# Optimization experiments

Hardware: AMD Instinct MI355X
Metric: run time of the kernel (lower is better)

The kernel has to match this reference:

```python
import jax, jax.numpy as jnp
import numpy as np

T, B, IN, H, F, OUT = 2048, 32, 256, 512, 2048, 256


def setup_inputs() -> dict:
    key = jax.random.key(0)
    ks = jax.random.split(key, 9)
    s_in = 1.0 / np.sqrt(IN)
    s_h = 1.0 / np.sqrt(H)
    s_f = 1.0 / np.sqrt(F)
    return {
        "x": jax.random.normal(ks[0], (T, B, IN), dtype=jnp.float32),
        "Wg": jax.random.uniform(ks[1], (H, IN), jnp.float32, -s_in, s_in),
        "bg": jax.random.uniform(ks[2], (H,), jnp.float32, -s_in, s_in),
        "Wi": jax.random.uniform(ks[3], (H, IN), jnp.float32, -s_in, s_in),
        "bi": jax.random.uniform(ks[4], (H,), jnp.float32, -s_in, s_in),
        "W1": jax.random.uniform(ks[5], (F, H), jnp.float32, -s_h, s_h),
        "b1": jax.random.uniform(ks[6], (F,), jnp.float32, -s_h, s_h),
        "W2": jax.random.uniform(ks[7], (OUT, F), jnp.float32, -s_f, s_f),
        "b2": jax.random.uniform(ks[8], (OUT,), jnp.float32, -s_f, s_f),
    }


def _gilr_scan(a, b):
    # h_t = a_t * h_{t-1} + b_t with h_0 = 0  ->  parallel associative scan over time
    def combine(c1, c2):
        a1, b1 = c1
        a2, b2 = c2
        return (a1 * a2, b1 * a2 + b2)
    _, h = jax.lax.associative_scan(combine, (a, b), axis=0)
    return h


def reference(x, Wg, bg, Wi, bi, W1, b1, W2, b2):
    # x: (T, B, IN)
    g = jax.nn.sigmoid(jnp.einsum("tbi,hi->tbh", x, Wg) + bg)  # (T,B,H)
    i = jnp.tanh(jnp.einsum("tbi,hi->tbh", x, Wi) + bi)        # (T,B,H)
    h = _gilr_scan(g, (1.0 - g) * i)                             # (T,B,H)
    z = jax.nn.gelu(jnp.einsum("tbh,fh->tbf", h, W1) + b1, approximate=False)
    out = jnp.einsum("tbf,of->tbo", z, W2) + b2                  # (T,B,OUT)
    return out
```

## Files before the change

kernel.cpp:

```cpp
#include <hip/hip_runtime.h>
#include <hip/hip_fp16.h>
#include <math.h>


#define T_DIM 2048
#define B_DIM 32
#define IN_DIM 256
#define H_DIM 512
#define F_DIM 2048
#define OUT_DIM 256

typedef _Float16 f16;
typedef _Float16 f16x8 __attribute__((ext_vector_type(8)));
typedef float f32x4 __attribute__((ext_vector_type(4)));

#define AS3(p) ((__attribute__((address_space(3))) void*)(p))
#define AS1(p) ((const __attribute__((address_space(1))) void*)(p))
#define MFMA16(d, x, y) d = __builtin_amdgcn_mfma_f32_16x16x32_f16(x, y, d, 0, 0, 0)


__global__ void cvt_kernel(const float* __restrict__ in, f16* __restrict__ out, int n8) {
  int i = blockIdx.x * blockDim.x + threadIdx.x;
  if (i >= n8) return;
  const float4* p = (const float4*)in + (size_t)i * 2;
  float4 a = p[0], b = p[1];
  f16x8 o = { (f16)a.x, (f16)a.y, (f16)a.z, (f16)a.w,
              (f16)b.x, (f16)b.y, (f16)b.z, (f16)b.w };
  *((f16x8*)out + i) = o;
}

__global__ void bias_cat_kernel(const float* __restrict__ bg, const float* __restrict__ bi,
                                float* __restrict__ bgi) {
  int t = threadIdx.x;
  bgi[t] = (t < 512) ? bg[t] : bi[t - 512];
}


template <int MODE, int LN, int MPX>
__global__ __launch_bounds__(256, 2) void gemm_bt(
    const f16* __restrict__ A, const f16* __restrict__ Bw,
    const float* __restrict__ bias, void* __restrict__ Cout,
    int lda, int ldb, int ldc, int K) {
  __shared__ f16 lds[2][2][128][64];
  const int tid = threadIdx.x;
  const int wid = tid >> 6, lane = tid & 63;
  const int bid = blockIdx.x;
  const int xcd = bid & 7, loc = bid >> 3;
  const int m0 = (xcd * MPX + (loc >> LN)) * 128;
  const int n0 = (loc & ((1 << LN) - 1)) * 128;
  const int wr = (wid >> 1) * 64;
  const int wc = (wid & 1) * 64;
  const int NT = K >> 6;

  auto stage = [&](int buf, int kt) {
    const f16* ga = A + (size_t)m0 * lda + kt * 64;
    const f16* gb = Bw + (size_t)n0 * ldb + kt * 64;
    f16* la = &lds[buf][0][0][0];
    f16* lb = &lds[buf][1][0][0];
#pragma unroll
    for (int q = 0; q < 4; ++q) {
      int seg = (wid << 2) + q;
      int s = seg * 64 + lane;
      int row = s >> 3, col = (s & 7) << 3;
      __builtin_amdgcn_global_load_lds(AS1(ga + (size_t)row * lda + col),
                                       AS3(la + seg * 512), 16, 0, 0);
      __builtin_amdgcn_global_load_lds(AS1(gb + (size_t)row * ldb + col),
                                       AS3(lb + seg * 512), 16, 0, 0);
    }
  };

  f32x4 acc[4][4] = {};
  stage(0, 0);
  for (int kt = 0; kt < NT; ++kt) {
    __syncthreads();
    if (kt + 1 < NT) stage((kt + 1) & 1, kt + 1);
    f16(*At)[64] = lds[kt & 1][0];
    f16(*Bt)[64] = lds[kt & 1][1];
    const int r = lane & 15, cg = (lane >> 4) << 3;
#pragma unroll
    for (int kk = 0; kk < 2; ++kk) {
      f16x8 af[4], bf[4];
#pragma unroll
      for (int i = 0; i < 4; ++i)
        af[i] = *(const f16x8*)&At[wr + i * 16 + r][kk * 32 + cg];
#pragma unroll
      for (int i = 0; i < 4; ++i)
        bf[i] = *(const f16x8*)&Bt[wc + i * 16 + r][kk * 32 + cg];
#pragma unroll
      for (int mi = 0; mi < 4; ++mi)
#pragma unroll
        for (int ni = 0; ni < 4; ++ni)
          acc[mi][ni] = __builtin_amdgcn_mfma_f32_16x16x32_f16(af[mi], bf[ni], acc[mi][ni], 0, 0, 0);
    }
  }

  const int r = lane & 15, rq = (lane >> 4) * 4;
#pragma unroll
  for (int ni = 0; ni < 4; ++ni) {
    int col = n0 + wc + ni * 16 + r;
    float bv = bias[col];
#pragma unroll
    for (int mi = 0; mi < 4; ++mi) {
#pragma unroll
      for (int j = 0; j < 4; ++j) {
        int row = m0 + wr + mi * 16 + rq + j;
        float v = acc[mi][ni][j] + bv;
        if constexpr (MODE == 2)
          ((float*)Cout)[(size_t)row * ldc + col] = v;
        else
          ((f16*)Cout)[(size_t)row * ldc + col] = (f16)v;
      }
    }
  }
}


__device__ __forceinline__ float gelu_fast(float v) {
  float u = v * v;
  float y = v * fmaf(0.0713548353f, u, 1.59576912161f);
  float e = __expf(-y);
  return v * __builtin_amdgcn_rcpf(1.0f + e);
}

__global__ __launch_bounds__(256, 2) void gemm2_f(
    const f16* __restrict__ A, const f16* __restrict__ Bw,
    const float* __restrict__ bias, f16* __restrict__ Cout) {
  constexpr int LDA = 1024, LDB = 512, LDC = 2048, K = 512, NT = K / 32;
  __shared__ f16 lds[3][384 * 32];
  const int tid = threadIdx.x, wid = tid >> 6, lane = tid & 63;
  const int lr = lane & 15;
  const int bid = blockIdx.x;
  const int m0 = ((bid & 7) * 8 + (bid >> 7)) * 256;
  const int n0 = ((bid >> 3) & 15) * 128;
  const int wr = (wid >> 1) * 128, wc = (wid & 1) * 64;

  const f16* srcA[4];
  const f16* srcB[2];
#pragma unroll
  for (int q = 0; q < 4; ++q) {
    int s = wid * 256 + q * 64 + lane;
    int row = s >> 2, g = (s & 3) ^ ((row + (row >> 2)) & 3);
    srcA[q] = A + (size_t)(m0 + row) * LDA + g * 8;
  }
#pragma unroll
  for (int q = 0; q < 2; ++q) {
    int s = wid * 128 + q * 64 + lane;
    int row = s >> 2, g = (s & 3) ^ ((row + (row >> 2)) & 3);
    srcB[q] = Bw + (size_t)(n0 + row) * LDB + g * 8;
  }

  auto stageA = [&](int buf, int kt) {
    f16* d = lds[buf] + wid * 2048;
#pragma unroll
    for (int q = 0; q < 4; ++q)
      __builtin_amdgcn_global_load_lds(AS1(srcA[q] + kt * 32), AS3(d + q * 512), 16, 0, 0);
  };
  auto stageB = [&](int buf, int kt) {
    f16* d = lds[buf] + 8192 + wid * 1024;
#pragma unroll
    for (int q = 0; q < 2; ++q)
      __builtin_amdgcn_global_load_lds(AS1(srcB[q] + kt * 32), AS3(d + q * 512), 16, 0, 0);
  };

  const int qsf = (((lane >> 4) ^ ((lr + (lr >> 2)) & 3)) << 3);
  auto fragA = [&](int buf, int mi) -> f16x8 {
    return *(const f16x8*)(lds[buf] + (wr + mi * 16 + lr) * 32 + qsf);
  };
  auto fragB = [&](int buf, int ni) -> f16x8 {
    return *(const f16x8*)(lds[buf] + 8192 + (wc + ni * 16 + lr) * 32 + qsf);
  };

  f32x4 acc[8][4] = {};
  stageA(0, 0); stageB(0, 0);
  stageA(1, 1); stageB(1, 1);
  asm volatile("s_waitcnt vmcnt(6)" ::: "memory");
  __builtin_amdgcn_s_barrier();

#pragma unroll
  for (int kt = 0; kt < NT; ++kt) {
    const int cur = kt % 3, nx2 = (kt + 2) % 3;
    f16x8 a[8], b[4];
#pragma unroll
    for (int mi = 0; mi < 8; ++mi) a[mi] = fragA(cur, mi);
    b[0] = fragB(cur, 0);
    b[1] = fragB(cur, 1);
    if (kt + 2 < NT) stageA(nx2, kt + 2);
    __builtin_amdgcn_s_barrier();
    asm volatile("s_waitcnt lgkmcnt(0)" ::: "memory");
    __builtin_amdgcn_sched_barrier(0);
    __builtin_amdgcn_s_setprio(1);
#pragma unroll
    for (int mi = 0; mi < 8; ++mi) { MFMA16(acc[mi][0], a[mi], b[0]); MFMA16(acc[mi][1], a[mi], b[1]); }
    __builtin_amdgcn_s_setprio(0);
    __builtin_amdgcn_s_barrier();
    b[2] = fragB(cur, 2);
    b[3] = fragB(cur, 3);
    if (kt + 2 < NT) stageB(nx2, kt + 2);
    __builtin_amdgcn_s_barrier();
    asm volatile("s_waitcnt lgkmcnt(0)" ::: "memory");
    __builtin_amdgcn_sched_barrier(0);
    __builtin_amdgcn_s_setprio(1);
#pragma unroll
    for (int mi = 0; mi < 8; ++mi) { MFMA16(acc[mi][2], a[mi], b[2]); MFMA16(acc[mi][3], a[mi], b[3]); }
    __builtin_amdgcn_s_setprio(0);
    if (kt + 2 < NT) asm volatile("s_waitcnt vmcnt(6)" ::: "memory");
    else             asm volatile("s_waitcnt vmcnt(0)" ::: "memory");
    __builtin_amdgcn_s_barrier();
  }

  __syncthreads();
  f16* ep = &lds[0][0] + wid * 8192;
  const int rq = (lane >> 4) * 4;
#pragma unroll
  for (int mi = 0; mi < 8; ++mi) {
#pragma unroll
    for (int ni = 0; ni < 4; ++ni) {
      int c = ni * 2 + (lr >> 3);
      float bv = bias[n0 + wc + ni * 16 + lr];
#pragma unroll
      for (int j = 0; j < 4; ++j) {
        int row = mi * 16 + rq + j;
        float v = gelu_fast(acc[mi][ni][j] + bv);
        ep[row * 64 + ((c ^ (row & 7)) << 3) + (lr & 7)] = (f16)v;
      }
    }
  }
  asm volatile("s_waitcnt lgkmcnt(0)" ::: "memory");
  __builtin_amdgcn_sched_barrier(0);
#pragma unroll
  for (int t = 0; t < 16; ++t) {
    int idx = t * 64 + lane;
    int row = idx >> 3, c = idx & 7;
    f16x8 v = *(const f16x8*)(ep + row * 64 + ((c ^ (row & 7)) << 3));
    *(f16x8*)(Cout + (size_t)(m0 + wr + row) * LDC + (n0 + wc) + c * 8) = v;
  }
}


#define NCH 16384
#define NCHUNK 32
#define CLEN 64

__global__ void scan_p1(const f16* __restrict__ ab, float* __restrict__ cA,
                        float* __restrict__ cH) {
  int ch = blockIdx.x * 256 + threadIdx.x;
  int c = blockIdx.y;
  const f16* pg = ab + (size_t)(c * CLEN) * 32768 + (ch >> 9) * 1024 + (ch & 511);
  const f16* pi = pg + 512;
  float A = 1.f, Hl = 0.f;
  for (int t = 0; t < CLEN; ++t) {
    float g = 1.f / (1.f + expf(-(float)pg[0]));
    float ii = tanhf((float)pi[0]);
    Hl = g * Hl + (1.f - g) * ii;
    A *= g;
    pg += 32768; pi += 32768;
  }
  cA[c * NCH + ch] = A;
  cH[c * NCH + ch] = Hl;
}

__global__ void scan_p2(const float* __restrict__ cA, const float* __restrict__ cH,
                        float* __restrict__ st) {
  int ch = blockIdx.x * 256 + threadIdx.x;
  float h0 = 0.f;
  for (int c = 0; c < NCHUNK; ++c) {
    st[c * NCH + ch] = h0;
    h0 = cA[c * NCH + ch] * h0 + cH[c * NCH + ch];
  }
}

__global__ void scan_p3(f16* __restrict__ ab, const float* __restrict__ st) {
  int ch = blockIdx.x * 256 + threadIdx.x;
  int c = blockIdx.y;
  f16* pg = ab + (size_t)(c * CLEN) * 32768 + (ch >> 9) * 1024 + (ch & 511);
  const f16* pi = pg + 512;
  float hv = st[c * NCH + ch];
  for (int t = 0; t < CLEN; ++t) {
    float g = 1.f / (1.f + expf(-(float)pg[0]));
    float ii = tanhf((float)pi[0]);
    hv = g * hv + (1.f - g) * ii;
    pg[0] = (f16)hv;
    pg += 32768; pi += 32768;
  }
}


extern "C" void kernel_launch(void* const* d_in, const int* in_sizes, int n_in,
                              void* d_out, int out_size, void* d_ws, size_t ws_size,
                              hipStream_t stream) {
  const float* x  = (const float*)d_in[0];
  const float* Wg = (const float*)d_in[1];
  const float* bg = (const float*)d_in[2];
  const float* Wi = (const float*)d_in[3];
  const float* bi = (const float*)d_in[4];
  const float* W1 = (const float*)d_in[5];
  const float* b1 = (const float*)d_in[6];
  const float* W2 = (const float*)d_in[7];
  const float* b2 = (const float*)d_in[8];
  float* out = (float*)d_out;

  char* ws = (char*)d_ws;
  f16*   wgi16 = (f16*)(ws + 0);
  f16*   w116  = (f16*)(ws + 524288);
  f16*   w216  = (f16*)(ws + 2621440);
  float* bgi   = (float*)(ws + 3670016);
  f16*   x16   = (f16*)(ws + 4194304);
  f16*   ab16  = (f16*)(ws + 37748736);
  float* cA    = (float*)(ws + 171966464);
  float* cH    = (float*)(ws + 174063616);
  float* st    = (float*)(ws + 176160768);
  f16*   z16   = (f16*)(ws + 178257920);
  if (ws_size < 245366784) return;

  cvt_kernel<<<64, 256, 0, stream>>>(Wg, wgi16, 16384);
  cvt_kernel<<<64, 256, 0, stream>>>(Wi, wgi16 + 131072, 16384);
  cvt_kernel<<<512, 256, 0, stream>>>(W1, w116, 131072);
  cvt_kernel<<<256, 256, 0, stream>>>(W2, w216, 65536);
  bias_cat_kernel<<<1, 1024, 0, stream>>>(bg, bi, bgi);
  cvt_kernel<<<8192, 256, 0, stream>>>(x, x16, 2097152);

  gemm_bt<0, 3, 64><<<4096, 256, 0, stream>>>(x16, wgi16, bgi, ab16,
                                              IN_DIM, IN_DIM, 1024, IN_DIM);

  scan_p1<<<dim3(64, NCHUNK), 256, 0, stream>>>(ab16, cA, cH);
  scan_p2<<<64, 256, 0, stream>>>(cA, cH, st);
  scan_p3<<<dim3(64, NCHUNK), 256, 0, stream>>>(ab16, st);

  for (int s = 0; s < 4; ++s) {
    const f16* hs = ab16 + (size_t)s * 16384 * 1024;
    gemm2_f<<<1024, 256, 0, stream>>>(hs, w116, b1, z16);
    gemm_bt<2, 1, 16><<<256, 256, 0, stream>>>(z16, w216, b2,
                                               out + (size_t)s * 16384 * 256,
                                               F_DIM, F_DIM, OUT_DIM, F_DIM);
  }
}
```

Measured before the change: 534.6 us.

## Fuse x conversion and gate activations into gemm1; add alternate gemm2 variant

```diff
diff --git a/kernel.cpp b/kernel.cpp
--- a/kernel.cpp
+++ b/kernel.cpp
@@ -35,26 +35,317 @@
   bgi[t] = (t < 512) ? bg[t] : bi[t - 512];
 }
 
-
-template <int MODE, int LN, int MPX>
-__global__ __launch_bounds__(256, 2) void gemm_bt(
+__device__ __forceinline__ float sigmoid_fast(float v) {
+  return __builtin_amdgcn_rcpf(1.0f + __expf(-v));
+}
+__device__ __forceinline__ float tanh_fast(float v) {
+  return 1.0f - 2.0f * __builtin_amdgcn_rcpf(__expf(2.0f * v) + 1.0f);
+}
+__device__ __forceinline__ float gelu_fast(float v) {
+  float u = v * v;
+  float y = v * fmaf(0.0713548353f, u, 1.59576912161f);
+  return v * __builtin_amdgcn_rcpf(1.0f + __expf(-y));
+}
+
+
+__global__ __launch_bounds__(256, 2) void gemm1_k(
+    const float* __restrict__ X, const f16* __restrict__ Bw,
+    const float* __restrict__ bias, f16* __restrict__ Cout) {
+  constexpr int NT = 4, LDA = 256, LDB = 256, LDC = 1024;
+  __shared__ f16 lds[2][2][128][64];
+  const int tid = threadIdx.x, wid = tid >> 6, lane = tid & 63;
+  const int bid = blockIdx.x;
+  const int m0 = ((bid & 7) * 64 + (bid >> 6)) * 128;
+  const int n0 = ((bid >> 3) & 7) * 128;
+  const int wr = (wid >> 1) * 64, wc = (wid & 1) * 64;
+
+  float4 sa[4][2];
+  auto loadA = [&](int kt) {
+#pragma unroll
+    for (int q = 0; q < 4; ++q) {
+      int s = tid * 4 + q, row = s >> 3, c = s & 7;
+      const float4* p = (const float4*)(X + (size_t)(m0 + row) * LDA + kt * 64 + c * 8);
+      sa[q][0] = p[0]; sa[q][1] = p[1];
+    }
+  };
+  auto writeA = [&](int buf) {
+#pragma unroll
+    for (int q = 0; q < 4; ++q) {
+      int s = tid * 4 + q, row = s >> 3, c = s & 7;
+      float4 a = sa[q][0], b = sa[q][1];
+      f16x8 o = { (f16)a.x, (f16)a.y, (f16)a.z, (f16)a.w,
+                  (f16)b.x, (f16)b.y, (f16)b.z, (f16)b.w };
+      *(f16x8*)&lds[buf][0][row][c * 8] = o;
+    }
+  };
+  auto stageB = [&](int buf, int kt) {
+    const f16* gb = Bw + (size_t)n0 * LDB + kt * 64;
+    f16* lb = &lds[buf][1][0][0];
+#pragma unroll
+    for (int q = 0; q < 4; ++q) {
+      int seg = (wid << 2) + q;
+      int s2 = seg * 64 + lane;
+      int row = s2 >> 3, col = (s2 & 7) << 3;
+      __builtin_amdgcn_global_load_lds(AS1(gb + (size_t)row * LDB + col),
+                                       AS3(lb + seg * 512), 16, 0, 0);
+    }
+  };
+
+  f32x4 acc[4][4] = {};
+  loadA(0); writeA(0); stageB(0, 0);
+  for (int kt = 0; kt < NT; ++kt) {
+    __syncthreads();
+    if (kt + 1 < NT) { loadA(kt + 1); stageB((kt + 1) & 1, kt + 1); }
+    f16(*At)[64] = lds[kt & 1][0];
+    f16(*Bt)[64] = lds[kt & 1][1];
+    const int r = lane & 15, cg = (lane >> 4) << 3;
+#pragma unroll
+    for (int kk = 0; kk < 2; ++kk) {
+      f16x8 af[4], bf[4];
+#pragma unroll
+      for (int i = 0; i < 4; ++i)
+        af[i] = *(const f16x8*)&At[wr + i * 16 + r][kk * 32 + cg];
+#pragma unroll
+      for (int i = 0; i < 4; ++i)
+        bf[i] = *(const f16x8*)&Bt[wc + i * 16 + r][kk * 32 + cg];
+#pragma unroll
+      for (int mi = 0; mi < 4; ++mi)
+#pragma unroll
+        for (int ni = 0; ni < 4; ++ni)
+          MFMA16(acc[mi][ni], af[mi], bf[ni]);
+    }
+    if (kt + 1 < NT) writeA((kt + 1) & 1);
+  }
+
+  __syncthreads();
+  f16* ep = &lds[0][0][0][0] + wid * 4096;
+  const int r = lane & 15, rq = (lane >> 4) * 4;
+#pragma unroll
+  for (int ni = 0; ni < 4; ++ni) {
+    int gcol = n0 + wc + ni * 16 + r;
+    float bv = bias[gcol];
+    bool sig = gcol < 512;
+    int cc = ni * 2 + (r >> 3);
+#pragma unroll
+    for (int mi = 0; mi < 4; ++mi) {
+#pragma unroll
+      for (int j = 0; j < 4; ++j) {
+        int lrow = mi * 16 + rq + j;
+        float v = acc[mi][ni][j] + bv;
+        float av = sig ? sigmoid_fast(v) : tanh_fast(v);
+        ep[lrow * 64 + ((cc ^ (lrow & 7)) << 3) + (r & 7)] = (f16)av;
+      }
+    }
+  }
+  asm volatile("s_waitcnt lgkmcnt(0)" ::: "memory");
+  __builtin_amdgcn_sched_barrier(0);
+#pragma unroll
+  for (int t = 0; t < 8; ++t) {
+    int idx = t * 64 + lane;
+    int row = idx >> 3, c = idx & 7;
+    f16x8 v = *(const f16x8*)(ep + row * 64 + ((c ^ (row & 7)) << 3));
+    *(f16x8*)(Cout + (size_t)(m0 + wr + row) * LDC + n0 + wc + c * 8) = v;
+  }
+}
+
+
+__global__ __launch_bounds__(256, 4) void gemm2_tlp(
     const f16* __restrict__ A, const f16* __restrict__ Bw,
-    const float* __restrict__ bias, void* __restrict__ Cout,
-    int lda, int ldb, int ldc, int K) {
+    const float* __restrict__ bias, f16* __restrict__ Cout) {
+  constexpr int LDA = 1024, LDB = 512, LDC = 2048, NT = 16;
+  __shared__ f16 lds[2][2][128][32];
+  const int tid = threadIdx.x, wid = tid >> 6, lane = tid & 63;
+  const int bid = blockIdx.x;
+  const int m0 = ((bid & 7) * 16 + (bid >> 7)) * 128;
+  const int n0 = ((bid >> 3) & 15) * 128;
+  const int wr = (wid >> 1) * 64, wc = (wid & 1) * 64;
+
+  const f16* srcA[2]; const f16* srcB[2];
+#pragma unroll
+  for (int q = 0; q < 2; ++q) {
+    int s = (wid * 2 + q) * 64 + lane;
+    int row = s >> 2, g = (s & 3) ^ ((row >> 1) & 3);
+    srcA[q] = A + (size_t)(m0 + row) * LDA + g * 8;
+    srcB[q] = Bw + (size_t)(n0 + row) * LDB + g * 8;
+  }
+  auto stage = [&](int buf, int kt) {
+    f16* la = &lds[buf][0][0][0] + (wid * 2) * 512;
+    f16* lb = &lds[buf][1][0][0] + (wid * 2) * 512;
+#pragma unroll
+    for (int q = 0; q < 2; ++q) {
+      __builtin_amdgcn_global_load_lds(AS1(srcA[q] + kt * 32), AS3(la + q * 512), 16, 0, 0);
+      __builtin_amdgcn_global_load_lds(AS1(srcB[q] + kt * 32), AS3(lb + q * 512), 16, 0, 0);
+    }
+  };
+  const int r = lane & 15;
+  const int cs = (((lane >> 4) ^ ((lane >> 1) & 3)) << 3);
+
+  f32x4 acc[4][4] = {};
+  stage(0, 0);
+  for (int kt = 0; kt < NT; ++kt) {
+    __syncthreads();
+    if (kt + 1 < NT) stage((kt + 1) & 1, kt + 1);
+    f16(*At)[32] = lds[kt & 1][0];
+    f16(*Bt)[32] = lds[kt & 1][1];
+    f16x8 af[4], bf[4];
+#pragma unroll
+    for (int i = 0; i < 4; ++i) af[i] = *(const f16x8*)&At[wr + i * 16 + r][cs];
+#pragma unroll
+    for (int i = 0; i < 4; ++i) bf[i] = *(const f16x8*)&Bt[wc + i * 16 + r][cs];
+#pragma unroll
+    for (int mi = 0; mi < 4; ++mi)
+#pragma unroll
+      for (int ni = 0; ni < 4; ++ni)
+        MFMA16(acc[mi][ni], af[mi], bf[ni]);
+  }
+
+  __syncthreads();
+  f16* ep = &lds[0][0][0][0] + wid * 4096;
+  const int rq = (lane >> 4) * 4;
+#pragma unroll
+  for (int ni = 0; ni < 4; ++ni) {
+    float bv = bias[n0 + wc + ni * 16 + r];
+    int cc = ni * 2 + (r >> 3);
+#pragma unroll
+    for (int mi = 0; mi < 4; ++mi) {
+#pragma unroll
+      for (int j = 0; j < 4; ++j) {
+        int lrow = mi * 16 + rq + j;
+        float v = gelu_fast(acc[mi][ni][j] + bv);
+        ep[lrow * 64 + ((cc ^ (lrow & 7)) << 3) + (r & 7)] = (f16)v;
+      }
+    }
+  }
+  asm volatile("s_waitcnt lgkmcnt(0)" ::: "memory");
+  __builtin_amdgcn_sched_barrier(0);
+#pragma unroll
+  for (int t = 0; t < 8; ++t) {
+    int idx = t * 64 + lane;
+    int row = idx >> 3, c = idx & 7;
+    f16x8 v = *(const f16x8*)(ep + row * 64 + ((c ^ (row & 7)) << 3));
+    *(f16x8*)(Cout + (size_t)(m0 + wr + row) * LDC + n0 + wc + c * 8) = v;
+  }
+}
+
+
+__global__ __launch_bounds__(256, 2) void gemm2_f(
+    const f16* __restrict__ A, const f16* __restrict__ Bw,
+    const float* __restrict__ bias, f16* __restrict__ Cout) {
+  constexpr int LDA = 1024, LDB = 512, LDC = 2048, NT = 16;
+  __shared__ f16 lds[3][384 * 32];
+  const int tid = threadIdx.x, wid = tid >> 6, lane = tid & 63;
+  const int lr = lane & 15;
+  const int bid = blockIdx.x;
+  const int m0 = ((bid & 7) * 8 + (bid >> 7)) * 256;
+  const int n0 = ((bid >> 3) & 15) * 128;
+  const int wr = (wid >> 1) * 128, wc = (wid & 1) * 64;
+
+  const f16* srcA[4];
+  const f16* srcB[2];
+#pragma unroll
+  for (int q = 0; q < 4; ++q) {
+    int s = wid * 256 + q * 64 + lane;
+    int row = s >> 2, g = (s & 3) ^ ((row + (row >> 2)) & 3);
+    srcA[q] = A + (size_t)(m0 + row) * LDA + g * 8;
+  }
+#pragma unroll
+  for (int q = 0; q < 2; ++q) {
+    int s = wid * 128 + q * 64 + lane;
+    int row = s >> 2, g = (s & 3) ^ ((row + (row >> 2)) & 3);
+    srcB[q] = Bw + (size_t)(n0 + row) * LDB + g * 8;
+  }
+  auto stageA = [&](int buf, int kt) {
+    f16* d = lds[buf] + wid * 2048;
+#pragma unroll
+    for (int q = 0; q < 4; ++q)
+      __builtin_amdgcn_global_load_lds(AS1(srcA[q] + kt * 32), AS3(d + q * 512), 16, 0, 0);
+  };
+  auto stageB = [&](int buf, int kt) {
+    f16* d = lds[buf] + 8192 + wid * 1024;
+#pragma unroll
+    for (int q = 0; q < 2; ++q)
+      __builtin_amdgcn_global_load_lds(AS1(srcB[q] + kt * 32), AS3(d + q * 512), 16, 0, 0);
+  };
+  const int qsf = (((lane >> 4) ^ ((lr + (lr >> 2)) & 3)) << 3);
+  auto fragA = [&](int buf, int mi) -> f16x8 {
+    return *(const f16x8*)(lds[buf] + (wr + mi * 16 + lr) * 32 + qsf);
+  };
+  auto fragB = [&](int buf, int ni) -> f16x8 {
+    return *(const f16x8*)(lds[buf] + 8192 + (wc + ni * 16 + lr) * 32 + qsf);
+  };
+
+  f32x4 acc[8][4] = {};
+  stageA(0, 0); stageB(0, 0);
+  stageA(1, 1); stageB(1, 1);
+  asm volatile("s_waitcnt vmcnt(6)" ::: "memory");
+  __builtin_amdgcn_s_barrier();
+
+#pragma unroll
+  for (int kt = 0; kt < NT; ++kt) {
+    const int cur = kt % 3, nx2 = (kt + 2) % 3;
+    f16x8 a[8], b[4];
+#pragma unroll
+    for (int mi = 0; mi < 8; ++mi) a[mi] = fragA(cur, mi);
+#pragma unroll
+    for (int ni = 0; ni < 4; ++ni) b[ni] = fragB(cur, ni);
+    if (kt + 2 < NT) { stageA(nx2, kt + 2); stageB(nx2, kt + 2); }
+    asm volatile("s_waitcnt lgkmcnt(0)" ::: "memory");
+    __builtin_amdgcn_sched_barrier(0);
+    __builtin_amdgcn_s_setprio(1);
+#pragma unroll
+    for (int mi = 0; mi < 8; ++mi) {
+      MFMA16(acc[mi][0], a[mi], b[0]); MFMA16(acc[mi][1], a[mi], b[1]);
+      MFMA16(acc[mi][2], a[mi], b[2]); MFMA16(acc[mi][3], a[mi], b[3]);
+    }
+    __builtin_amdgcn_s_setprio(0);
+    if (kt + 2 < NT) asm volatile("s_waitcnt vmcnt(6)" ::: "memory");
+    else             asm volatile("s_waitcnt vmcnt(0)" ::: "memory");
+    __builtin_amdgcn_s_barrier();
+  }
+
+  __syncthreads();
+  f16* ep = &lds[0][0] + wid * 8192;
+  const int rq = (lane >> 4) * 4;
+#pragma unroll
+  for (int mi = 0; mi < 8; ++mi) {
+#pragma unroll
+    for (int ni = 0; ni < 4; ++ni) {
+      int c = ni * 2 + (lr >> 3);
+      float bv = bias[n0 + wc + ni * 16 + lr];
+#pragma unroll
+      for (int j = 0; j < 4; ++j) {
+        int row = mi * 16 + rq + j;
+        float v = gelu_fast(acc[mi][ni][j] + bv);
+        ep[row * 64 + ((c ^ (row & 7)) << 3) + (lr & 7)] = (f16)v;
+      }
+    }
+  }
+  asm volatile("s_waitcnt lgkmcnt(0)" ::: "memory");
+  __builtin_amdgcn_sched_barrier(0);
+#pragma unroll
+  for (int t = 0; t < 16; ++t) {
+    int idx = t * 64 + lane;
+    int row = idx >> 3, c = idx & 7;
+    f16x8 v = *(const f16x8*)(ep + row * 64 + ((c ^ (row & 7)) << 3));
+    *(f16x8*)(Cout + (size_t)(m0 + wr + row) * LDC + (n0 + wc) + c * 8) = v;
+  }
+}
+
+
+__global__ __launch_bounds__(256, 2) void gemm3_k(
+    const f16* __restrict__ A, const f16* __restrict__ Bw,
+    const float* __restrict__ bias, float* __restrict__ Cout) {
+  constexpr int LDA = 2048, LDB = 2048, LDC = 256, NT = 32;
   __shared__ f16 lds[2][2][128][64];
-  const int tid = threadIdx.x;
-  const int wid = tid >> 6, lane = tid & 63;
+  const int tid = threadIdx.x, wid = tid >> 6, lane = tid & 63;
   const int bid = blockIdx.x;
-  const int xcd = bid & 7, loc = bid >> 3;
-  const int m0 = (xcd * MPX + (loc >> LN)) * 128;
-  const int n0 = (loc & ((1 << LN) - 1)) * 128;
-  const int wr = (wid >> 1) * 64;
-  const int wc = (wid & 1) * 64;
-  const int NT = K >> 6;
+  const int m0 = ((bid & 7) * 16 + (bid >> 4)) * 128;
+  const int n0 = ((bid >> 3) & 1) * 128;
+  const int wr = (wid >> 1) * 64, wc = (wid & 1) * 64;
 
   auto stage = [&](int buf, int kt) {
-    const f16* ga = A + (size_t)m0 * lda + kt * 64;
-    const f16* gb = Bw + (size_t)n0 * ldb + kt * 64;
+    const f16* ga = A + (size_t)m0 * LDA + kt * 64;
+    const f16* gb = Bw + (size_t)n0 * LDB + kt * 64;
     f16* la = &lds[buf][0][0][0];
     f16* lb = &lds[buf][1][0][0];
 #pragma unroll
@@ -62,9 +353,9 @@
       int seg = (wid << 2) + q;
       int s = seg * 64 + lane;
       int row = s >> 3, col = (s & 7) << 3;
-      __builtin_amdgcn_global_load_lds(AS1(ga + (size_t)row * lda + col),
+      __builtin_amdgcn_global_load_lds(AS1(ga + (size_t)row * LDA + col),
                                        AS3(la + seg * 512), 16, 0, 0);
-      __builtin_amdgcn_global_load_lds(AS1(gb + (size_t)row * ldb + col),
+      __builtin_amdgcn_global_load_lds(AS1(gb + (size_t)row * LDB + col),
                                        AS3(lb + seg * 512), 16, 0, 0);
     }
   };
@@ -90,10 +381,9 @@
       for (int mi = 0; mi < 4; ++mi)
 #pragma unroll
         for (int ni = 0; ni < 4; ++ni)
-          acc[mi][ni] = __builtin_amdgcn_mfma_f32_16x16x32_f16(af[mi], bf[ni], acc[mi][ni], 0, 0, 0);
-    }
-  }
-
+          MFMA16(acc[mi][ni], af[mi], bf[ni]);
+    }
+  }
   const int r = lane & 15, rq = (lane >> 4) * 4;
 #pragma unroll
   for (int ni = 0; ni < 4; ++ni) {
@@ -104,135 +394,9 @@
 #pragma unroll
       for (int j = 0; j < 4; ++j) {
         int row = m0 + wr + mi * 16 + rq + j;
-        float v = acc[mi][ni][j] + bv;
-        if constexpr (MODE == 2)
-          ((float*)Cout)[(size_t)row * ldc + col] = v;
-        else
-          ((f16*)Cout)[(size_t)row * ldc + col] = (f16)v;
+        Cout[(size_t)row * LDC + col] = acc[mi][ni][j] + bv;
       }
     }
-  }
-}
-
-
-__device__ __forceinline__ float gelu_fast(float v) {
-  float u = v * v;
-  float y = v * fmaf(0.0713548353f, u, 1.59576912161f);
-  float e = __expf(-y);
-  return v * __builtin_amdgcn_rcpf(1.0f + e);
-}
-
-__global__ __launch_bounds__(256, 2) void gemm2_f(
-    const f16* __restrict__ A, const f16* __restrict__ Bw,
-    const float* __restrict__ bias, f16* __restrict__ Cout) {
-  constexpr int LDA = 1024, LDB = 512, LDC = 2048, K = 512, NT = K / 32;
-  __shared__ f16 lds[3][384 * 32];
-  const int tid = threadIdx.x, wid = tid >> 6, lane = tid & 63;
-  const int lr = lane & 15;
-  const int bid = blockIdx.x;
-  const int m0 = ((bid & 7) * 8 + (bid >> 7)) * 256;
-  const int n0 = ((bid >> 3) & 15) * 128;
-  const int wr = (wid >> 1) * 128, wc = (wid & 1) * 64;
-
-  const f16* srcA[4];
-  const f16* srcB[2];
-#pragma unroll
-  for (int q = 0; q < 4; ++q) {
-    int s = wid * 256 + q * 64 + lane;
-    int row = s >> 2, g = (s & 3) ^ ((row + (row >> 2)) & 3);
-    srcA[q] = A + (size_t)(m0 + row) * LDA + g * 8;
-  }
-#pragma unroll
-  for (int q = 0; q < 2; ++q) {
-    int s = wid * 128 + q * 64 + lane;
-    int row = s >> 2, g = (s & 3) ^ ((row + (row >> 2)) & 3);
-    srcB[q] = Bw + (size_t)(n0 + row) * LDB + g * 8;
-  }
-
-  auto stageA = [&](int buf, int kt) {
-    f16* d = lds[buf] + wid * 2048;
-#pragma unroll
-    for (int q = 0; q < 4; ++q)
-      __builtin_amdgcn_global_load_lds(AS1(srcA[q] + kt * 32), AS3(d + q * 512), 16, 0, 0);
-  };
-  auto stageB = [&](int buf, int kt) {
-    f16* d = lds[buf] + 8192 + wid * 1024;
-#pragma unroll
-    for (int q = 0; q < 2; ++q)
-      __builtin_amdgcn_global_load_lds(AS1(srcB[q] + kt * 32), AS3(d + q * 512), 16, 0, 0);
-  };
-
-  const int qsf = (((lane >> 4) ^ ((lr + (lr >> 2)) & 3)) << 3);
-  auto fragA = [&](int buf, int mi) -> f16x8 {
-    return *(const f16x8*)(lds[buf] + (wr + mi * 16 + lr) * 32 + qsf);
-  };
-  auto fragB = [&](int buf, int ni) -> f16x8 {
-    return *(const f16x8*)(lds[buf] + 8192 + (wc + ni * 16 + lr) * 32 + qsf);
-  };
-
-  f32x4 acc[8][4] = {};
-  stageA(0, 0); stageB(0, 0);
-  stageA(1, 1); stageB(1, 1);
-  asm volatile("s_waitcnt vmcnt(6)" ::: "memory");
-  __builtin_amdgcn_s_barrier();
-
-#pragma unroll
-  for (int kt = 0; kt < NT; ++kt) {
-    const int cur = kt % 3, nx2 = (kt + 2) % 3;
-    f16x8 a[8], b[4];
-#pragma unroll
-    for (int mi = 0; mi < 8; ++mi) a[mi] = fragA(cur, mi);
-    b[0] = fragB(cur, 0);
-    b[1] = fragB(cur, 1);
-    if (kt + 2 < NT) stageA(nx2, kt + 2);
-    __builtin_amdgcn_s_barrier();
-    asm volatile("s_waitcnt lgkmcnt(0)" ::: "memory");
-    __builtin_amdgcn_sched_barrier(0);
-    __builtin_amdgcn_s_setprio(1);
-#pragma unroll
-    for (int mi = 0; mi < 8; ++mi) { MFMA16(acc[mi][0], a[mi], b[0]); MFMA16(acc[mi][1], a[mi], b[1]); }
-    __builtin_amdgcn_s_setprio(0);
-    __builtin_amdgcn_s_barrier();
-    b[2] = fragB(cur, 2);
-    b[3] = fragB(cur, 3);
-    if (kt + 2 < NT) stageB(nx2, kt + 2);
-    __builtin_amdgcn_s_barrier();
-    asm volatile("s_waitcnt lgkmcnt(0)" ::: "memory");
-    __builtin_amdgcn_sched_barrier(0);
-    __builtin_amdgcn_s_setprio(1);
-#pragma unroll
-    for (int mi = 0; mi < 8; ++mi) { MFMA16(acc[mi][2], a[mi], b[2]); MFMA16(acc[mi][3], a[mi], b[3]); }
-    __builtin_amdgcn_s_setprio(0);
-    if (kt + 2 < NT) asm volatile("s_waitcnt vmcnt(6)" ::: "memory");
-    else             asm volatile("s_waitcnt vmcnt(0)" ::: "memory");
-    __builtin_amdgcn_s_barrier();
-  }
-
-  __syncthreads();
-  f16* ep = &lds[0][0] + wid * 8192;
-  const int rq = (lane >> 4) * 4;
-#pragma unroll
-  for (int mi = 0; mi < 8; ++mi) {
-#pragma unroll
-    for (int ni = 0; ni < 4; ++ni) {
-      int c = ni * 2 + (lr >> 3);
-      float bv = bias[n0 + wc + ni * 16 + lr];
-#pragma unroll
-      for (int j = 0; j < 4; ++j) {
-        int row = mi * 16 + rq + j;
-        float v = gelu_fast(acc[mi][ni][j] + bv);
-        ep[row * 64 + ((c ^ (row & 7)) << 3) + (lr & 7)] = (f16)v;
-      }
-    }
-  }
-  asm volatile("s_waitcnt lgkmcnt(0)" ::: "memory");
-  __builtin_amdgcn_sched_barrier(0);
-#pragma unroll
-  for (int t = 0; t < 16; ++t) {
-    int idx = t * 64 + lane;
-    int row = idx >> 3, c = idx & 7;
-    f16x8 v = *(const f16x8*)(ep + row * 64 + ((c ^ (row & 7)) << 3));
-    *(f16x8*)(Cout + (size_t)(m0 + wr + row) * LDC + (n0 + wc) + c * 8) = v;
   }
 }
 
@@ -249,9 +413,9 @@
   const f16* pi = pg + 512;
   float A = 1.f, Hl = 0.f;
   for (int t = 0; t < CLEN; ++t) {
-    float g = 1.f / (1.f + expf(-(float)pg[0]));
-    float ii = tanhf((float)pi[0]);
-    Hl = g * Hl + (1.f - g) * ii;
+    float g = (float)pg[0];
+    float ii = (float)pi[0];
+    Hl = fmaf(g, Hl - ii, ii);
     A *= g;
     pg += 32768; pi += 32768;
   }
@@ -276,9 +440,9 @@
   const f16* pi = pg + 512;
   float hv = st[c * NCH + ch];
   for (int t = 0; t < CLEN; ++t) {
-    float g = 1.f / (1.f + expf(-(float)pg[0]));
-    float ii = tanhf((float)pi[0]);
-    hv = g * hv + (1.f - g) * ii;
+    float g = (float)pg[0];
+    float ii = (float)pi[0];
+    hv = fmaf(g, hv - ii, ii);
     pg[0] = (f16)hv;
     pg += 32768; pi += 32768;
   }
@@ -304,7 +468,6 @@
   f16*   w116  = (f16*)(ws + 524288);
   f16*   w216  = (f16*)(ws + 2621440);
   float* bgi   = (float*)(ws + 3670016);
-  f16*   x16   = (f16*)(ws + 4194304);
   f16*   ab16  = (f16*)(ws + 37748736);
   float* cA    = (float*)(ws + 171966464);
   float* cH    = (float*)(ws + 174063616);
@@ -317,10 +480,8 @@
   cvt_kernel<<<512, 256, 0, stream>>>(W1, w116, 131072);
   cvt_kernel<<<256, 256, 0, stream>>>(W2, w216, 65536);
   bias_cat_kernel<<<1, 1024, 0, stream>>>(bg, bi, bgi);
-  cvt_kernel<<<8192, 256, 0, stream>>>(x, x16, 2097152);
-
-  gemm_bt<0, 3, 64><<<4096, 256, 0, stream>>>(x16, wgi16, bgi, ab16,
-                                              IN_DIM, IN_DIM, 1024, IN_DIM);
+
+  gemm1_k<<<4096, 256, 0, stream>>>(x, wgi16, bgi, ab16);
 
   scan_p1<<<dim3(64, NCHUNK), 256, 0, stream>>>(ab16, cA, cH);
   scan_p2<<<64, 256, 0, stream>>>(cA, cH, st);
@@ -328,9 +489,10 @@
 
   for (int s = 0; s < 4; ++s) {
     const f16* hs = ab16 + (size_t)s * 16384 * 1024;
-    gemm2_f<<<1024, 256, 0, stream>>>(hs, w116, b1, z16);
-    gemm_bt<2, 1, 16><<<256, 256, 0, stream>>>(z16, w216, b2,
-                                               out + (size_t)s * 16384 * 256,
-                                               F_DIM, F_DIM, OUT_DIM, F_DIM);
-  }
-}
+    if (s < 2)
+      gemm2_tlp<<<2048, 256, 0, stream>>>(hs, w116, b1, z16);
+    else
+      gemm2_f<<<1024, 256, 0, stream>>>(hs, w116, b1, z16);
+    gemm3_k<<<256, 256, 0, stream>>>(z16, w216, b2, out + (size_t)s * 16384 * 256);
+  }
+}
```

Result: slower. 563.0 us (+5.3%).
